# Performance work log

Hardware: AMD Instinct MI355X
Metric: run time of the kernel (lower is better)

## Reference

```python
import jax, jax.numpy as jnp
import numpy as np

B, S, H = 2, 2048, 2048
NH, NKV, HD = 16, 4, 128
GROUPS = NH // NKV
THETA = 10000.0
EPS = 1e-6


def setup_inputs() -> dict:
    key = jax.random.key(0)
    ks = jax.random.split(key, 6)
    scale = 0.02
    return {
        "hidden_states": jax.random.normal(ks[0], (B, S, H), jnp.float32),
        "wq": jax.random.normal(ks[1], (NH * HD, H), jnp.float32) * scale,
        "wk": jax.random.normal(ks[2], (NKV * HD, H), jnp.float32) * scale,
        "wv": jax.random.normal(ks[3], (NKV * HD, H), jnp.float32) * scale,
        "wo": jax.random.normal(ks[4], (H, NH * HD), jnp.float32) * scale,
        "q_norm_weight": jnp.ones((HD,), jnp.float32),
        "k_norm_weight": jnp.ones((HD,), jnp.float32),
    }


def _rope_tables(seq_len):
    inv_freq = 1.0 / (THETA ** (jnp.arange(0, HD, 2, dtype=jnp.float32) / HD))
    t = jnp.arange(seq_len, dtype=jnp.float32)
    freqs = jnp.outer(t, inv_freq)              # [S, HD/2]
    emb = jnp.concatenate([freqs, freqs], -1)   # [S, HD]
    return jnp.cos(emb), jnp.sin(emb)


def _rotate_half(x):
    x1, x2 = x[..., : HD // 2], x[..., HD // 2:]
    return jnp.concatenate([-x2, x1], -1)


def _rmsnorm(x, w):
    var = jnp.mean(jnp.square(x), axis=-1, keepdims=True)
    return x * jax.lax.rsqrt(var + EPS) * w


def reference(hidden_states, wq, wk, wv, wo, q_norm_weight, k_norm_weight):
    b, s, _ = hidden_states.shape
    q = (hidden_states @ wq.T).reshape(b, s, NH, HD).transpose(0, 2, 1, 3)    # [b,nh,s,d]
    k = (hidden_states @ wk.T).reshape(b, s, NKV, HD).transpose(0, 2, 1, 3)   # [b,nkv,s,d]
    v = (hidden_states @ wv.T).reshape(b, s, NKV, HD).transpose(0, 2, 1, 3)

    cos, sin = _rope_tables(s)                  # [s,d]
    q = q * cos + _rotate_half(q) * sin
    k = k * cos + _rotate_half(k) * sin

    # fused QK RMSNorm (applied inside fused_qknorm_flash_attention)
    q = _rmsnorm(q, q_norm_weight)
    k = _rmsnorm(k, k_norm_weight)

    # GQA: share each kv head across GROUPS query heads without materializing repeats
    qg = q.reshape(b, NKV, GROUPS, s, HD)
    scale = 1.0 / jnp.sqrt(jnp.float32(HD))
    scores = jnp.einsum('bhgqd,bhkd->bhgqk', qg, k) * scale   # [b,nkv,g,s,s]
    causal = jnp.tril(jnp.ones((s, s), bool))
    scores = jnp.where(causal, scores, jnp.finfo(scores.dtype).min)
    probs = jax.nn.softmax(scores, axis=-1)
    out = jnp.einsum('bhgqk,bhkd->bhgqd', probs, v)            # [b,nkv,g,s,d]
    out = out.reshape(b, NH, s, HD).transpose(0, 2, 1, 3).reshape(b, s, NH * HD)
    return out @ wo.T
```

## Files before the change

kernel.cpp:

```cpp
#include <hip/hip_runtime.h>
#include <math.h>

typedef __bf16 bf16;
typedef __bf16 bf16x8 __attribute__((ext_vector_type(8)));
typedef __bf16 bf16x4 __attribute__((ext_vector_type(4)));
typedef float f32x4 __attribute__((ext_vector_type(4)));

#define B_DIM 2
#define S_LEN 2048
#define H_DIM 2048
#define NH 16
#define NKV 4
#define HD 128

__device__ __forceinline__ void gl_lds16(const void* g, void* l) {
    __builtin_amdgcn_global_load_lds(
        (const __attribute__((address_space(1))) unsigned int*)g,
        (__attribute__((address_space(3))) unsigned int*)l, 16, 0, 0);
}

__device__ __forceinline__ void bar() {
    asm volatile("" ::: "memory");
    __builtin_amdgcn_s_barrier();
    asm volatile("" ::: "memory");
}

__global__ __launch_bounds__(256) void cast_all(const float* __restrict__ s0,
                                                const float* __restrict__ s1,
                                                const float* __restrict__ s2,
                                                const float* __restrict__ s3,
                                                const float* __restrict__ s4,
                                                bf16* __restrict__ dst) {
    const int i = blockIdx.x * 256 + threadIdx.x;
    const float* src;
    int off;
    if (i < 2097152)      { src = s0; off = 0; }
    else if (i < 3145728) { src = s1; off = 2097152; }
    else if (i < 3407872) { src = s2; off = 3145728; }
    else if (i < 3670016) { src = s3; off = 3407872; }
    else                  { src = s4; off = 3670016; }
    float4 f = ((const float4*)src)[i - off];
    bf16x4 o = { (bf16)f.x, (bf16)f.y, (bf16)f.z, (bf16)f.w };
    *(bf16x4*)(dst + (size_t)i * 4) = o;
}

template <typename OutT>
__global__ __launch_bounds__(512, 2) void gemm256(const bf16* __restrict__ A,
                                                  const bf16* __restrict__ Bt,
                                                  OutT* __restrict__ C,
                                                  int M, int N, int K) {
    __shared__ __align__(16) bf16 smem[65536];
    const int t = threadIdx.x, lane = t & 63, w = t >> 6;
    const int lr = lane & 15, quad = lane >> 4;
    const int nN = N >> 8;
    const int nwg = gridDim.x, chunk = nwg >> 3;
    const int bid = blockIdx.x;
    const int lid = (bid & 7) * chunk + (bid >> 3);
    const int m0 = (lid / nN) << 8, n0 = (lid % nN) << 8;
    const int mh_w = w >> 2;
    const int wn = (w & 3) << 6;
    const int nh_w = (w & 3) >> 1;
    const int rb = (w & 1) << 6;
    const int nK = K >> 6;
    const int nIter = K >> 7;

    const int ld0 = w * 2;
    const int lrow = lane >> 2;
    const int csrc = (lane & 3) ^ ((lane >> 5) << 1);
    const int swz = (lr >> 3) << 1;

    auto stA = [&](int ts, int mh) {
        if (ts < nK) {
            bf16* db = smem + (ts & 1) * 16384 + mh * 8192;
            const bf16* sp = A + (size_t)(m0 + mh * 128) * K + ts * 64;
#pragma unroll
            for (int i = 0; i < 2; i++) {
                const int ldi = ld0 + i, kb = ldi >> 3, rg = ldi & 7;
                gl_lds16(sp + (size_t)(rg * 16 + lrow) * K + kb * 32 + csrc * 8,
                         db + kb * 4096 + rg * 512);
            }
        }
    };
    auto stB = [&](int ts, int nh) {
        if (ts < nK) {
            bf16* db = smem + 32768 + (ts & 1) * 16384 + nh * 8192;
            const bf16* sp = Bt + (size_t)(n0 + nh * 128) * K + ts * 64;
#pragma unroll
            for (int i = 0; i < 2; i++) {
                const int ldi = ld0 + i, kb = ldi >> 3, rg = ldi & 7;
                gl_lds16(sp + (size_t)(rg * 16 + lrow) * K + kb * 32 + csrc * 8,
                         db + kb * 4096 + rg * 512);
            }
        }
    };

    f32x4 acc[8][4];
#pragma unroll
    for (int i = 0; i < 8; i++)
#pragma unroll
        for (int j = 0; j < 4; j++) acc[i][j] = (f32x4){0.f, 0.f, 0.f, 0.f};
    bf16x8 af[8], b0[4], b1[4];

    auto rdA = [&](int s, int fi0) {
        const bf16* bp = smem + s * 16384 + mh_w * 8192;
#pragma unroll
        for (int f = 0; f < 4; f++)
#pragma unroll
            for (int ks = 0; ks < 2; ks++)
                af[f * 2 + ks] = *(const bf16x8*)(bp + ks * 4096 +
                                                  ((fi0 + f) * 16 + lr) * 32 + (quad ^ swz) * 8);
    };
    auto rdB = [&](int s, int fj0, bf16x8* dst) {
        const bf16* bp = smem + 32768 + s * 16384 + nh_w * 8192;
#pragma unroll
        for (int f = 0; f < 2; f++)
#pragma unroll
            for (int ks = 0; ks < 2; ks++)
                dst[f * 2 + ks] = *(const bf16x8*)(bp + ks * 4096 +
                                                   (rb + (fj0 + f) * 16 + lr) * 32 + (quad ^ swz) * 8);
    };
    auto mm16 = [&](int fi0, int fj0, bf16x8* bb) {
        __builtin_amdgcn_s_setprio(1);
#pragma unroll
        for (int f = 0; f < 4; f++)
#pragma unroll
            for (int g = 0; g < 2; g++)
#pragma unroll
                for (int ks = 0; ks < 2; ks++)
                    acc[fi0 + f][fj0 + g] = __builtin_amdgcn_mfma_f32_16x16x32_bf16(
                        af[f * 2 + ks], bb[g * 2 + ks], acc[fi0 + f][fj0 + g], 0, 0, 0);
        __builtin_amdgcn_s_setprio(0);
    };

    stA(0, 0); stA(0, 1); stB(0, 0); stB(0, 1); stA(1, 0);
    asm volatile("s_waitcnt vmcnt(2)" ::: "memory");
    bar();

    for (int i = 0; i < nIter; i++) {
        const int ts0 = 2 * i;
#pragma unroll
        for (int h = 0; h < 2; h++) {
            const int ts = ts0 + h, s = h;
            rdA(s, 0); rdB(s, 0, b0);
            stA(ts + 1, 1);
            bar();
            mm16(0, 0, b0);
            bar();
            rdB(s, 2, b1);
            stB(ts + 1, 0);
            bar();
            mm16(0, 2, b1);
            bar();
            rdA(s, 4);
            stB(ts + 1, 1);
            bar();
            mm16(4, 2, b1);
            bar();
            rdB(s, 0, b0);
            stA(ts + 2, 0);
            bar();
            mm16(4, 0, b0);
            if (ts + 2 < nK) asm volatile("s_waitcnt vmcnt(2)" ::: "memory");
            else             asm volatile("s_waitcnt vmcnt(0)" ::: "memory");
            bar();
        }
    }
#pragma unroll
    for (int fi = 0; fi < 8; fi++) {
        const int m = m0 + mh_w * 128 + fi * 16 + quad * 4;
#pragma unroll
        for (int fj = 0; fj < 4; fj++) {
            const int n = n0 + wn + fj * 16 + lr;
#pragma unroll
            for (int r = 0; r < 4; r++)
                C[(size_t)(m + r) * N + n] = (OutT)acc[fi][fj][r];
        }
    }
}

__global__ __launch_bounds__(256) void rope_rms(const bf16* __restrict__ qkv,
                                                const float* __restrict__ qw,
                                                const float* __restrict__ kw,
                                                bf16* __restrict__ qb,
                                                bf16* __restrict__ kb,
                                                bf16* __restrict__ vt) {
    const int tok = blockIdx.x;
    const int b = tok >> 11, s = tok & (S_LEN - 1);
    const int lane = threadIdx.x & 63, w = threadIdx.x >> 6;
    const bf16* row = qkv + (size_t)tok * 3072;
    const float inv = expf(-(float)lane * (9.210340371976184f / 64.f));
    const float ang = (float)s * inv;
    float s_, c_;
    sincosf(ang, &s_, &c_);
    const float wq1 = qw[lane], wq2 = qw[lane + 64];
    const float wk1 = kw[lane], wk2 = kw[lane + 64];
    for (int u = w; u < 24; u += 4) {
        if (u < 16) {
            const float x1 = (float)row[u * 128 + lane], x2 = (float)row[u * 128 + 64 + lane];
            float y1 = x1 * c_ - x2 * s_;
            float y2 = x2 * c_ + x1 * s_;
            float ss = y1 * y1 + y2 * y2;
#pragma unroll
            for (int m = 1; m < 64; m <<= 1) ss += __shfl_xor(ss, m);
            const float r = rsqrtf(ss * (1.f / 128.f) + 1e-6f);
            size_t o = ((size_t)(b * NH + u) * S_LEN + s) * HD;
            qb[o + lane]      = (bf16)(y1 * r * wq1);
            qb[o + 64 + lane] = (bf16)(y2 * r * wq2);
        } else if (u < 20) {
            const int kh = u - 16;
            const float x1 = (float)row[2048 + kh * 128 + lane], x2 = (float)row[2048 + kh * 128 + 64 + lane];
            float y1 = x1 * c_ - x2 * s_;
            float y2 = x2 * c_ + x1 * s_;
            float ss = y1 * y1 + y2 * y2;
#pragma unroll
            for (int m = 1; m < 64; m <<= 1) ss += __shfl_xor(ss, m);
            const float r = rsqrtf(ss * (1.f / 128.f) + 1e-6f);
            size_t base = (size_t)(b * NKV + kh) * 16 * 16384;
            kb[base + (size_t)(lane >> 3) * 16384 + s * 8 + (lane & 7)]       = (bf16)(y1 * r * wk1);
            kb[base + (size_t)(8 + (lane >> 3)) * 16384 + s * 8 + (lane & 7)] = (bf16)(y2 * r * wk2);
        } else {
            const int vh = u - 20;
            const float x1 = (float)row[2560 + vh * 128 + lane], x2 = (float)row[2560 + vh * 128 + 64 + lane];
            const int m = s & 31;
            const int gi = (s >> 5) * 4 + ((m & 15) >> 2);
            const int el = ((m >> 4) << 2) | (m & 3);
            size_t base = ((size_t)(b * NKV + vh) * 256 + gi) * 1024 + el;
            vt[base + (size_t)lane * 8]        = (bf16)x1;
            vt[base + (size_t)(lane + 64) * 8] = (bf16)x2;
        }
    }
}

__global__ __launch_bounds__(256, 2) void flash(const bf16* __restrict__ qg,
                                                const bf16* __restrict__ kg,
                                                const bf16* __restrict__ vg,
                                                bf16* __restrict__ attn) {
    const int idx = blockIdx.x;
    const int g = idx >> 5;
    const int qt = (g < 8) ? (15 - g) : (g - 8);
    const int hb = idx & 31;
    const int h = hb & 15, b = hb >> 4;
    const int kvh = h >> 2;
    const bf16* qh = qg + (size_t)(b * NH + h) * S_LEN * HD;
    const bf16* kh = kg + (size_t)(b * NKV + kvh) * (16 * 16384);
    const bf16* vh = vg + (size_t)(b * NKV + kvh) * (256 * 1024);
    __shared__ __align__(16) bf16 Ks[2][16 * 512];
    __shared__ __align__(16) bf16 Vs[2][8 * 1024];
    const int t = threadIdx.x, lane = t & 63, w = t >> 6, lr = lane & 15, quad = lane >> 4;
    const int row0 = qt * 128 + w * 32;
    bf16x8 qf[2][4];
#pragma unroll
    for (int mg = 0; mg < 2; mg++)
#pragma unroll
        for (int c = 0; c < 4; c++)
            qf[mg][c] = *(const bf16x8*)(qh + (size_t)(row0 + mg * 16 + lr) * HD + c * 32 + quad * 8);
    f32x4 o[2][8];
    f32x4 lacc[2];
#pragma unroll
    for (int mg = 0; mg < 2; mg++) {
        lacc[mg] = (f32x4){0.f, 0.f, 0.f, 0.f};
#pragma unroll
        for (int j = 0; j < 8; j++) o[mg][j] = (f32x4){0.f, 0.f, 0.f, 0.f};
    }
    const bf16 one = (bf16)1.0f;
    const bf16x8 ones8 = {one, one, one, one, one, one, one, one};
    const float C1 = 0.12751744f;
    const float C2 = -17.3123405f;
    const int ntile = 2 * qt + 2;

    auto stage = [&](int kt_, int bi) {
        const int kb = kt_ * 64;
#pragma unroll
        for (int i = 0; i < 4; i++) {
            const int dc = w * 4 + i;
            gl_lds16(kh + (size_t)dc * 16384 + (size_t)kb * 8 + lane * 8, &Ks[bi][dc * 512]);
        }
#pragma unroll
        for (int i = 0; i < 2; i++) {
            const int c = w * 2 + i;
            const bf16* src = vh + (size_t)(8 * kt_ + ((c >> 2) << 2) + (c & 3)) * 1024 + lane * 8;
            gl_lds16(src, &Vs[bi][c * 1024]);
            gl_lds16(src + 512, &Vs[bi][c * 1024 + 512]);
        }
    };

    stage(0, 0);
    __syncthreads();
    int cur = 0;

    for (int kt = 0; kt < ntile; ++kt) {
        const int kbase = kt * 64;
        if (kt + 1 < ntile) stage(kt + 1, cur ^ 1);
        f32x4 sacc[2][4];
#pragma unroll
        for (int mg = 0; mg < 2; mg++)
#pragma unroll
            for (int n = 0; n < 4; n++) sacc[mg][n] = (f32x4){0.f, 0.f, 0.f, 0.f};
#pragma unroll
        for (int n = 0; n < 4; n++)
#pragma unroll
            for (int c = 0; c < 4; c++) {
                bf16x8 kf = *(const bf16x8*)&Ks[cur][(c * 4 + quad) * 512 + (n * 16 + lr) * 8];
                sacc[0][n] = __builtin_amdgcn_mfma_f32_16x16x32_bf16(kf, qf[0][c], sacc[0][n], 0, 0, 0);
                sacc[1][n] = __builtin_amdgcn_mfma_f32_16x16x32_bf16(kf, qf[1][c], sacc[1][n], 0, 0, 0);
            }
        const bool diag = (kt >= 2 * qt);
        bf16x8 pT[2][2];
#pragma unroll
        for (int mg = 0; mg < 2; mg++) {
            const int qrow = row0 + mg * 16 + lr;
#pragma unroll
            for (int n = 0; n < 4; n++)
#pragma unroll
                for (int r = 0; r < 4; r++) {
                    float ev = exp2f(fmaf(sacc[mg][n][r], C1, C2));
                    if (diag) {
                        const int key = kbase + n * 16 + quad * 4 + r;
                        ev = (key <= qrow) ? ev : 0.f;
                    }
                    pT[mg][n >> 1][(n & 1) * 4 + r] = (bf16)ev;
                }
        }
#pragma unroll
        for (int k2 = 0; k2 < 2; k2++) {
#pragma unroll
            for (int j = 0; j < 8; j++) {
                bf16x8 vf = *(const bf16x8*)&Vs[cur][(k2 * 4 + quad) * 1024 + (j * 16 + lr) * 8];
                o[0][j] = __builtin_amdgcn_mfma_f32_16x16x32_bf16(vf, pT[0][k2], o[0][j], 0, 0, 0);
                o[1][j] = __builtin_amdgcn_mfma_f32_16x16x32_bf16(vf, pT[1][k2], o[1][j], 0, 0, 0);
            }
            lacc[0] = __builtin_amdgcn_mfma_f32_16x16x32_bf16(ones8, pT[0][k2], lacc[0], 0, 0, 0);
            lacc[1] = __builtin_amdgcn_mfma_f32_16x16x32_bf16(ones8, pT[1][k2], lacc[1], 0, 0, 0);
        }
        __syncthreads();
        cur ^= 1;
    }
#pragma unroll
    for (int mg = 0; mg < 2; mg++) {
        const float inv = 1.0f / lacc[mg][0];
        const int qrow = row0 + mg * 16 + lr;
        bf16* dst = attn + ((size_t)(b * S_LEN) + qrow) * (NH * HD) + h * HD + quad * 4;
#pragma unroll
        for (int j = 0; j < 8; j++) {
            bf16x4 st = { (bf16)(o[mg][j][0] * inv), (bf16)(o[mg][j][1] * inv),
                          (bf16)(o[mg][j][2] * inv), (bf16)(o[mg][j][3] * inv) };
            *(bf16x4*)(dst + j * 16) = st;
        }
    }
}

extern "C" void kernel_launch(void* const* d_in, const int* in_sizes, int n_in,
                              void* d_out, int out_size, void* d_ws, size_t ws_size,
                              hipStream_t stream) {
    (void)in_sizes; (void)n_in; (void)out_size; (void)ws_size;
    const float* hs  = (const float*)d_in[0];
    const float* wq  = (const float*)d_in[1];
    const float* wk  = (const float*)d_in[2];
    const float* wv  = (const float*)d_in[3];
    const float* wo  = (const float*)d_in[4];
    const float* qnw = (const float*)d_in[5];
    const float* knw = (const float*)d_in[6];
    float* out = (float*)d_out;

    char* ws = (char*)d_ws;
    size_t off = 0;
    auto alloc = [&](size_t bytes) {
        void* p = ws + off;
        off += (bytes + 255) & ~(size_t)255;
        return p;
    };
    bf16* hs_bf   = (bf16*)alloc((size_t)4096 * 2048 * 2);
    bf16* wqkv_bf = (bf16*)alloc((size_t)3072 * 2048 * 2);
    bf16* wo_bf   = (bf16*)alloc((size_t)2048 * 2048 * 2);
    bf16* qkv_bf  = (bf16*)alloc((size_t)4096 * 3072 * 2);
    bf16* q_bf    = (bf16*)alloc((size_t)B_DIM * NH * S_LEN * HD * 2);
    bf16* k_bf    = (bf16*)alloc((size_t)B_DIM * NKV * S_LEN * HD * 2);
    bf16* vt_bf   = (bf16*)alloc((size_t)B_DIM * NKV * S_LEN * HD * 2);
    bf16* at_bf   = (bf16*)alloc((size_t)4096 * 2048 * 2);

    cast_all<<<18432, 256, 0, stream>>>(hs, wq, wk, wv, wo, hs_bf);
    gemm256<bf16><<<dim3(192), 512, 0, stream>>>(hs_bf, wqkv_bf, qkv_bf, 4096, 3072, 2048);
    rope_rms<<<4096, 256, 0, stream>>>(qkv_bf, qnw, knw, q_bf, k_bf, vt_bf);
    flash<<<dim3(512), 256, 0, stream>>>(q_bf, k_bf, vt_bf, at_bf);
    gemm256<float><<<dim3(128), 512, 0, stream>>>(at_bf, wo_bf, out, 4096, 2048, 2048);
}
```

Baseline: 321.5 us.

## Split long causal query tiles across two blocks and reduce partials

Query tiles 10-15 have their key range split into two halves, each processed by its own block. The blocks write unnormalized fp32 partial outputs and row sums into the reused hidden-state buffer, and a new reduce kernel combines them. This balances work across the 704 blocks and tail, and occupancy rises to 3 blocks per CU by single-buffering V with an explicit barrier between score and PV. The GEMM LDS swizzle pattern also changes. The cost is an extra kernel launch, the partial-result memory traffic, and an added barrier per iteration.

```diff
diff --git a/kernel.cpp b/kernel.cpp
--- a/kernel.cpp
+++ b/kernel.cpp
@@ -66,8 +66,8 @@
 
     const int ld0 = w * 2;
     const int lrow = lane >> 2;
-    const int csrc = (lane & 3) ^ ((lane >> 5) << 1);
-    const int swz = (lr >> 3) << 1;
+    const int csrc = (lane & 3) ^ ((lane >> 3) & 3);
+    const int swz = (lr >> 1) & 3;
 
     auto stA = [&](int ts, int mh) {
         if (ts < nK) {
@@ -231,21 +231,26 @@
     }
 }
 
-__global__ __launch_bounds__(256, 2) void flash(const bf16* __restrict__ qg,
+__global__ __launch_bounds__(256, 3) void flash(const bf16* __restrict__ qg,
                                                 const bf16* __restrict__ kg,
                                                 const bf16* __restrict__ vg,
-                                                bf16* __restrict__ attn) {
+                                                bf16* __restrict__ attn,
+                                                float* __restrict__ part_o,
+                                                float* __restrict__ part_l) {
+    static const unsigned char QT[22] = {9,8,15,15,7,14,14,13,13,6,12,12,11,11,5,10,10,4,3,2,1,0};
+    static const unsigned char CK[22] = {2,2,0,1,2,0,1,0,1,2,0,1,0,1,2,0,1,2,2,2,2,2};
     const int idx = blockIdx.x;
-    const int g = idx >> 5;
-    const int qt = (g < 8) ? (15 - g) : (g - 8);
-    const int hb = idx & 31;
+    const int g = idx >> 5, hb = idx & 31;
+    const int qt = QT[g], ck = CK[g];
     const int h = hb & 15, b = hb >> 4;
     const int kvh = h >> 2;
+    const int ktBeg = (ck == 1) ? (qt + 1) : 0;
+    const int ktEnd = (ck == 0) ? (qt + 1) : (2 * qt + 2);
     const bf16* qh = qg + (size_t)(b * NH + h) * S_LEN * HD;
     const bf16* kh = kg + (size_t)(b * NKV + kvh) * (16 * 16384);
     const bf16* vh = vg + (size_t)(b * NKV + kvh) * (256 * 1024);
     __shared__ __align__(16) bf16 Ks[2][16 * 512];
-    __shared__ __align__(16) bf16 Vs[2][8 * 1024];
+    __shared__ __align__(16) bf16 Vs[8 * 1024];
     const int t = threadIdx.x, lane = t & 63, w = t >> 6, lr = lane & 15, quad = lane >> 4;
     const int row0 = qt * 128 + w * 32;
     bf16x8 qf[2][4];
@@ -266,31 +271,36 @@
     const bf16x8 ones8 = {one, one, one, one, one, one, one, one};
     const float C1 = 0.12751744f;
     const float C2 = -17.3123405f;
-    const int ntile = 2 * qt + 2;
-
-    auto stage = [&](int kt_, int bi) {
-        const int kb = kt_ * 64;
-#pragma unroll
-        for (int i = 0; i < 4; i++) {
-            const int dc = w * 4 + i;
-            gl_lds16(kh + (size_t)dc * 16384 + (size_t)kb * 8 + lane * 8, &Ks[bi][dc * 512]);
-        }
+
+    auto stageK = [&](int kt_) {
+        if (kt_ < ktEnd) {
+            bf16* dst = Ks[kt_ & 1];
+            const int kb = kt_ * 64;
+#pragma unroll
+            for (int i = 0; i < 4; i++) {
+                const int dc = w * 4 + i;
+                gl_lds16(kh + (size_t)dc * 16384 + (size_t)kb * 8 + lane * 8, dst + dc * 512);
+            }
+        }
+    };
+    auto stageV = [&](int kt_) {
 #pragma unroll
         for (int i = 0; i < 2; i++) {
             const int c = w * 2 + i;
-            const bf16* src = vh + (size_t)(8 * kt_ + ((c >> 2) << 2) + (c & 3)) * 1024 + lane * 8;
-            gl_lds16(src, &Vs[bi][c * 1024]);
-            gl_lds16(src + 512, &Vs[bi][c * 1024 + 512]);
-        }
-    };
-
-    stage(0, 0);
+            const bf16* src = vh + (size_t)(8 * kt_ + c) * 1024 + lane * 8;
+            gl_lds16(src, &Vs[c * 1024]);
+            gl_lds16(src + 512, &Vs[c * 1024 + 512]);
+        }
+    };
+
+    stageK(ktBeg);
+    stageK(ktBeg + 1);
     __syncthreads();
-    int cur = 0;
-
-    for (int kt = 0; kt < ntile; ++kt) {
+
+    for (int kt = ktBeg; kt < ktEnd; ++kt) {
         const int kbase = kt * 64;
-        if (kt + 1 < ntile) stage(kt + 1, cur ^ 1);
+        const int cur = kt & 1;
+        stageV(kt);
         f32x4 sacc[2][4];
 #pragma unroll
         for (int mg = 0; mg < 2; mg++)
@@ -321,31 +331,72 @@
                     pT[mg][n >> 1][(n & 1) * 4 + r] = (bf16)ev;
                 }
         }
+        asm volatile("s_waitcnt vmcnt(0)" ::: "memory");
+        bar();
+        stageK(kt + 2);
 #pragma unroll
         for (int k2 = 0; k2 < 2; k2++) {
 #pragma unroll
             for (int j = 0; j < 8; j++) {
-                bf16x8 vf = *(const bf16x8*)&Vs[cur][(k2 * 4 + quad) * 1024 + (j * 16 + lr) * 8];
+                bf16x8 vf = *(const bf16x8*)&Vs[(k2 * 4 + quad) * 1024 + (j * 16 + lr) * 8];
                 o[0][j] = __builtin_amdgcn_mfma_f32_16x16x32_bf16(vf, pT[0][k2], o[0][j], 0, 0, 0);
                 o[1][j] = __builtin_amdgcn_mfma_f32_16x16x32_bf16(vf, pT[1][k2], o[1][j], 0, 0, 0);
             }
             lacc[0] = __builtin_amdgcn_mfma_f32_16x16x32_bf16(ones8, pT[0][k2], lacc[0], 0, 0, 0);
             lacc[1] = __builtin_amdgcn_mfma_f32_16x16x32_bf16(ones8, pT[1][k2], lacc[1], 0, 0, 0);
         }
-        __syncthreads();
-        cur ^= 1;
-    }
-#pragma unroll
-    for (int mg = 0; mg < 2; mg++) {
-        const float inv = 1.0f / lacc[mg][0];
-        const int qrow = row0 + mg * 16 + lr;
-        bf16* dst = attn + ((size_t)(b * S_LEN) + qrow) * (NH * HD) + h * HD + quad * 4;
-#pragma unroll
-        for (int j = 0; j < 8; j++) {
-            bf16x4 st = { (bf16)(o[mg][j][0] * inv), (bf16)(o[mg][j][1] * inv),
-                          (bf16)(o[mg][j][2] * inv), (bf16)(o[mg][j][3] * inv) };
-            *(bf16x4*)(dst + j * 16) = st;
-        }
+        bar();
+    }
+    if (ck == 2) {
+#pragma unroll
+        for (int mg = 0; mg < 2; mg++) {
+            const float inv = 1.0f / lacc[mg][0];
+            const int qrow = row0 + mg * 16 + lr;
+            bf16* dst = attn + ((size_t)(b * S_LEN) + qrow) * (NH * HD) + h * HD + quad * 4;
+#pragma unroll
+            for (int j = 0; j < 8; j++) {
+                bf16x4 st = { (bf16)(o[mg][j][0] * inv), (bf16)(o[mg][j][1] * inv),
+                              (bf16)(o[mg][j][2] * inv), (bf16)(o[mg][j][3] * inv) };
+                *(bf16x4*)(dst + j * 16) = st;
+            }
+        }
+    } else {
+        const int slot = ((b * NH + h) * 6 + (qt - 10)) * 2 + ck;
+        float* po = part_o + (size_t)slot * 16384;
+#pragma unroll
+        for (int mg = 0; mg < 2; mg++) {
+            const int row = w * 32 + mg * 16 + lr;
+#pragma unroll
+            for (int j = 0; j < 8; j++) {
+                float4 st = { o[mg][j][0], o[mg][j][1], o[mg][j][2], o[mg][j][3] };
+                *(float4*)(po + row * 128 + j * 16 + quad * 4) = st;
+            }
+            if (quad == 0) part_l[slot * 128 + row] = lacc[mg][0];
+        }
+    }
+}
+
+__global__ __launch_bounds__(256) void reduce_attn(const float* __restrict__ part_o,
+                                                   const float* __restrict__ part_l,
+                                                   bf16* __restrict__ attn) {
+    const int blk = blockIdx.x;
+    const int qt = (blk % 6) + 10;
+    const int h = (blk / 6) & 15, b = blk / 96;
+    const float* p0 = part_o + (size_t)(blk * 2 + 0) * 16384;
+    const float* p1 = part_o + (size_t)(blk * 2 + 1) * 16384;
+    const float* l0 = part_l + (blk * 2 + 0) * 128;
+    const float* l1 = part_l + (blk * 2 + 1) * 128;
+    const int t = threadIdx.x;
+#pragma unroll
+    for (int it = 0; it < 16; it++) {
+        const int idx = it * 256 + t;
+        const int row = idx >> 5, d4 = idx & 31;
+        float4 a = ((const float4*)p0)[idx];
+        float4 c = ((const float4*)p1)[idx];
+        const float inv = 1.0f / (l0[row] + l1[row]);
+        bf16x4 ov = { (bf16)((a.x + c.x) * inv), (bf16)((a.y + c.y) * inv),
+                      (bf16)((a.z + c.z) * inv), (bf16)((a.w + c.w) * inv) };
+        *(bf16x4*)(attn + ((size_t)(b * S_LEN) + qt * 128 + row) * (NH * HD) + h * HD + d4 * 4) = ov;
     }
 }
 
@@ -378,9 +429,13 @@
     bf16* vt_bf   = (bf16*)alloc((size_t)B_DIM * NKV * S_LEN * HD * 2);
     bf16* at_bf   = (bf16*)alloc((size_t)4096 * 2048 * 2);
 
+    float* part_o = (float*)hs_bf;
+    float* part_l = (float*)((char*)hs_bf + (size_t)384 * 16384 * 4);
+
     cast_all<<<18432, 256, 0, stream>>>(hs, wq, wk, wv, wo, hs_bf);
     gemm256<bf16><<<dim3(192), 512, 0, stream>>>(hs_bf, wqkv_bf, qkv_bf, 4096, 3072, 2048);
     rope_rms<<<4096, 256, 0, stream>>>(qkv_bf, qnw, knw, q_bf, k_bf, vt_bf);
-    flash<<<dim3(512), 256, 0, stream>>>(q_bf, k_bf, vt_bf, at_bf);
+    flash<<<dim3(704), 256, 0, stream>>>(q_bf, k_bf, vt_bf, at_bf, part_o, part_l);
+    reduce_attn<<<dim3(192), 256, 0, stream>>>(part_o, part_l, at_bf);
     gemm256<float><<<dim3(128), 512, 0, stream>>>(at_bf, wo_bf, out, 4096, 2048, 2048);
 }
```

Result: faster. 313.2 us (-2.6%).
